# Kernel optimization log

Measured on AMD Instinct MI355X. Metric: run time of the kernel, lower is better.

Reference implementation:

```python
import jax, jax.numpy as jnp
import numpy as np

B, S, D = 1, 2048, 2048
H, G, HD = 32, 8, 64        # n_heads, n_kv_groups, head_dim
GS = H // G                  # group_size
ROPE_BASE = 10000.0


def _rope_tables(seq_len, head_dim):
    inv_freq = 1.0 / (ROPE_BASE ** (jnp.arange(0, head_dim, 2, dtype=jnp.float32) / head_dim))
    angles = jnp.arange(seq_len, dtype=jnp.float32)[:, None] * inv_freq[None, :]  # [S, HD/2]
    angles = jnp.concatenate([angles, angles], axis=-1)                            # [S, HD]
    return jnp.cos(angles), jnp.sin(angles)


def setup_inputs() -> dict:
    key = jax.random.key(0)
    ks = jax.random.split(key, 5)
    x = jax.random.normal(ks[0], (B, S, D), dtype=jnp.float32)
    mask = jnp.triu(jnp.ones((S, S), dtype=bool), k=1)  # True = masked (causal)
    cos_vals, sin_vals = _rope_tables(S, HD)
    scale = 0.02
    Wq = jax.random.normal(ks[1], (H * HD, D), dtype=jnp.float32) * scale
    Wk = jax.random.normal(ks[2], (G * HD, D), dtype=jnp.float32) * scale
    Wv = jax.random.normal(ks[3], (G * HD, D), dtype=jnp.float32) * scale
    Wo = jax.random.normal(ks[4], (D, H * HD), dtype=jnp.float32) * scale
    return {"x": x, "mask": mask, "cos_vals": cos_vals, "sin_vals": sin_vals,
            "Wq": Wq, "Wk": Wk, "Wv": Wv, "Wo": Wo}


def _apply_rope(t, cos, sin):
    # t: [b, heads, S, HD]; cos/sin: [S, HD]
    half = t.shape[-1] // 2
    t1, t2 = t[..., :half], t[..., half:]
    rotated = jnp.concatenate([-t2, t1], axis=-1)
    return t * cos[None, None] + rotated * sin[None, None]


def reference(x, mask, cos_vals, sin_vals, Wq, Wk, Wv, Wo):
    b, s, _ = x.shape
    q = (x @ Wq.T).reshape(b, s, H, HD).transpose(0, 2, 1, 3)   # [b,H,S,HD]
    k = (x @ Wk.T).reshape(b, s, G, HD).transpose(0, 2, 1, 3)   # [b,G,S,HD]
    v = (x @ Wv.T).reshape(b, s, G, HD).transpose(0, 2, 1, 3)   # [b,G,S,HD]
    q = _apply_rope(q, cos_vals, sin_vals)
    k = _apply_rope(k, cos_vals, sin_vals)
    # Group-broadcast instead of repeat_interleave (same math)
    q = q.reshape(b, G, GS, s, HD)
    scores = jnp.einsum('bghqd,bgkd->bghqk', q, k)              # [b,G,GS,S,S]
    scores = jnp.where(mask[None, None, None], -jnp.inf, scores)
    weights = jax.nn.softmax(scores / np.sqrt(HD).astype(np.float32), axis=-1)
    out = jnp.einsum('bghqk,bgkd->bghqd', weights, v)           # [b,G,GS,S,HD]
    out = out.reshape(b, H, s, HD).transpose(0, 2, 1, 3).reshape(b, s, H * HD)
    return out @ Wo.T
```

## Files before the change

### kernel.cpp

```cpp
#include <hip/hip_runtime.h>
#include <cstddef>
#include <cstdint>

#define S 2048
#define Dm 2048
#define NH 32
#define NG 8
#define HD 64

typedef __attribute__((ext_vector_type(8))) short bf16x8;
typedef __attribute__((ext_vector_type(4))) short bf16x4;
typedef __attribute__((ext_vector_type(4))) float f32x4;

__device__ __forceinline__ float fast_exp2(float x) { return __builtin_amdgcn_exp2f(x); }

__device__ __forceinline__ unsigned short f2bf(float f) {
  unsigned int u = __builtin_bit_cast(unsigned int, f);
  u = (u + 0x7fffu + ((u >> 16) & 1u)) >> 16;
  return (unsigned short)u;
}
__device__ __forceinline__ unsigned int pk2bf(float lo, float hi) {
  unsigned int a = __builtin_bit_cast(unsigned int, lo) + 0x8000u;
  unsigned int b = __builtin_bit_cast(unsigned int, hi) + 0x8000u;
  return (a >> 16) | (b & 0xffff0000u);
}
__device__ __forceinline__ void gl_lds16(const unsigned short* g, unsigned short* l) {
  __builtin_amdgcn_global_load_lds(
      (const __attribute__((address_space(1))) unsigned int*)g,
      (__attribute__((address_space(3))) unsigned int*)l, 16, 0, 0);
}

__device__ __forceinline__ void lds_drain_barrier() {
  asm volatile("s_waitcnt lgkmcnt(0)" ::: "memory");
  asm volatile("s_barrier" ::: "memory");
}

#define QSC 0.1803368801111601f

__global__ __launch_bounds__(256) void cvt_all(const float* __restrict__ x,
                                               const float* __restrict__ Wq,
                                               const float* __restrict__ Wk,
                                               const float* __restrict__ Wv,
                                               const float* __restrict__ Wo,
                                               unsigned short* __restrict__ xb,
                                               unsigned short* __restrict__ Wcat,
                                               unsigned short* __restrict__ Wob) {
  int i = blockIdx.x * 256 + threadIdx.x;
  const float4* src;
  ushort4* dst;
  if (i < 1048576)      { src = (const float4*)x  + i;             dst = (ushort4*)xb + i; }
  else if (i < 2097152) { src = (const float4*)Wq + (i - 1048576); dst = (ushort4*)Wcat + (i - 1048576); }
  else if (i < 2359296) { src = (const float4*)Wk + (i - 2097152); dst = (ushort4*)Wcat + 1048576 + (i - 2097152); }
  else if (i < 2621440) { src = (const float4*)Wv + (i - 2359296); dst = (ushort4*)Wcat + 1310720 + (i - 2359296); }
  else                  { src = (const float4*)Wo + (i - 2621440); dst = (ushort4*)Wob + (i - 2621440); }
  float4 v = *src;
  ushort4 o;
  o.x = f2bf(v.x); o.y = f2bf(v.y); o.z = f2bf(v.z); o.w = f2bf(v.w);
  *dst = o;
}

template<int MI, int NJ>
__global__ __launch_bounds__(256) void gemm_bf16(const unsigned short* __restrict__ A,
                                                 const unsigned short* __restrict__ B,
                                                 float* __restrict__ Cf,
                                                 unsigned short* __restrict__ Cb,
                                                 unsigned short* __restrict__ VtOut,
                                                 const float* __restrict__ cosv,
                                                 const float* __restrict__ sinv,
                                                 int M, int N, int K) {
  constexpr int BM = MI * 32, BN = NJ * 32;
  __shared__ __align__(16) unsigned short As[2][BM * 64];
  __shared__ __align__(16) unsigned short Bs[2][BN * 64];
  const int tid = threadIdx.x;
  const int lane = tid & 63, wave = tid >> 6;
  const int row0 = blockIdx.y * BM, col0 = blockIdx.x * BN;
  const int wr = (wave >> 1) * (MI * 16), wc = (wave & 1) * (NJ * 16);
  const int fr = lane & 15, q4 = lane >> 4;

  f32x4 acc[MI][NJ];
#pragma unroll
  for (int i = 0; i < MI; i++)
#pragma unroll
    for (int j = 0; j < NJ; j++) acc[i][j] = (f32x4){0.f, 0.f, 0.f, 0.f};

  const int nk = K >> 6;

  auto stage = [&](int k0, int buf) {
#pragma unroll
    for (int c = 0; c < MI; c++) {
      int p = tid + c * 256;
      int r = p >> 3, sl = ((p & 7) ^ (r & 7)) * 8;
      gl_lds16(&A[(size_t)(row0 + r) * K + k0 + sl], &As[buf][p * 8]);
    }
#pragma unroll
    for (int b = 0; b < NJ; b++) {
      int p = tid + b * 256;
      int r = p >> 3, sl = ((p & 7) ^ (r & 7)) * 8;
      gl_lds16(&B[(size_t)(col0 + r) * K + k0 + sl], &Bs[buf][p * 8]);
    }
  };

  auto compute = [&](const unsigned short* Ab, const unsigned short* Bb) {
#pragma unroll
    for (int kk = 0; kk < 2; kk++) {
      bf16x8 af[MI], bfr[NJ];
#pragma unroll
      for (int i = 0; i < MI; i++) {
        int R = wr + i * 16 + fr;
        af[i] = *(const bf16x8*)&Ab[R * 64 + ((q4 + kk * 4) ^ (R & 7)) * 8];
      }
#pragma unroll
      for (int j = 0; j < NJ; j++) {
        int R = wc + j * 16 + fr;
        bfr[j] = *(const bf16x8*)&Bb[R * 64 + ((q4 + kk * 4) ^ (R & 7)) * 8];
      }
#pragma unroll
      for (int i = 0; i < MI; i++)
#pragma unroll
        for (int j = 0; j < NJ; j++)
          acc[i][j] = __builtin_amdgcn_mfma_f32_16x16x32_bf16(af[i], bfr[j], acc[i][j], 0, 0, 0);
    }
  };

  stage(0, 0);
  stage(64, 1);

  for (int t = 0; t < nk; ++t) {
    if (t + 1 < nk) {
      if constexpr (MI + NJ == 6)      asm volatile("s_waitcnt vmcnt(6)" ::: "memory");
      else if constexpr (MI + NJ == 4) asm volatile("s_waitcnt vmcnt(4)" ::: "memory");
      else                             asm volatile("s_waitcnt vmcnt(8)" ::: "memory");
    } else {
      asm volatile("s_waitcnt vmcnt(0)" ::: "memory");
    }
    asm volatile("s_barrier" ::: "memory");

    compute(As[t & 1], Bs[t & 1]);

    lds_drain_barrier();
    if (t + 2 < nk) stage((t + 2) << 6, t & 1);
  }

  const int cc = lane & 15, cr = (lane >> 4) * 4;

  if (cosv) {
#pragma unroll
    for (int i = 0; i < MI; i++) {
      int grb = row0 + wr + i * 16 + cr;
#pragma unroll
      for (int j = 0; j < 2; j++) {
        int gc = col0 + wc + j * 16 + cc;
        if (gc < 2560) {
          int d = j * 16 + cc;
          float qs = (gc < 2048) ? QSC : 1.0f;
#pragma unroll
          for (int r = 0; r < 4; r++) {
            float c = cosv[(grb + r) * 64 + d];
            float s = sinv[(grb + r) * 64 + d];
            float t1 = acc[i][j][r], t2 = acc[i][j + 2][r];
            acc[i][j][r]     = (t1 * c - t2 * s) * qs;
            acc[i][j + 2][r] = (t2 * c + t1 * s) * qs;
          }
        }
      }
    }
  }

#pragma unroll
  for (int i = 0; i < MI; i++)
#pragma unroll
    for (int j = 0; j < NJ; j++) {
      int gc = col0 + wc + j * 16 + cc;
#pragma unroll
      for (int r = 0; r < 4; r++) {
        int gr = row0 + wr + i * 16 + cr + r;
        if (cosv) {
          if (gc >= 2560) VtOut[(size_t)(gc - 2560) * 2048 + gr] = f2bf(acc[i][j][r]);
          else            Cb[(size_t)gr * N + gc] = f2bf(acc[i][j][r]);
        } else if (Cf)    Cf[(size_t)gr * N + gc] = acc[i][j][r];
        else              Cb[(size_t)gr * N + gc] = f2bf(acc[i][j][r]);
      }
    }
}

__global__ __launch_bounds__(256, 2) void flash_mfma(const unsigned short* __restrict__ QKV,
                                                     const unsigned short* __restrict__ Vt_g,
                                                     unsigned short* __restrict__ Ob) {
  __shared__ __align__(16) unsigned short Ks[2][64 * 64];
  __shared__ __align__(16) unsigned short Vs[2][64 * 64];

  const int tid = threadIdx.x;
  const int lane = tid & 63, wave = tid >> 6;
  const int m15 = lane & 15, q4 = lane >> 4;

  const int L = blockIdx.x;
  const int h = L & 31, g = h >> 2;
  const int u0 = L >> 5, a = u0 >> 3, b = u0 & 7;
  const int u = (a == 0) ? 15 - b : b;
  const int qb = u * 128;
  const int ntiles = 2 * u + 2;

  bf16x8 qf[2][2];
#pragma unroll
  for (int f = 0; f < 2; f++) {
    const size_t qrow = (size_t)(qb + f * 64 + wave * 16 + m15) * 3072 + h * 64;
    qf[f][0] = *(const bf16x8*)&QKV[qrow + q4 * 8];
    qf[f][1] = *(const bf16x8*)&QKV[qrow + 32 + q4 * 8];
  }

  f32x4 accO[2][4];
  float l_lane[2] = {0.f, 0.f};
#pragma unroll
  for (int f = 0; f < 2; f++)
#pragma unroll
    for (int v = 0; v < 4; v++) accO[f][v] = (f32x4){0.f, 0.f, 0.f, 0.f};

  const int p0 = wave * 128 + lane, p1 = p0 + 64;
  const int sr0 = p0 >> 3, so0 = ((p0 & 7) ^ (sr0 & 7)) * 8;
  const int sr1 = p1 >> 3, so1 = ((p1 & 7) ^ (sr1 & 7)) * 8;

#pragma unroll
  for (int t = 0; t < 2; t++) {
    const int k0 = t * 64;
    gl_lds16(&QKV[(size_t)(k0 + sr0) * 3072 + 2048 + g * 64 + so0], &Ks[t][p0 * 8]);
    gl_lds16(&QKV[(size_t)(k0 + sr1) * 3072 + 2048 + g * 64 + so1], &Ks[t][p1 * 8]);
    gl_lds16(&Vt_g[(size_t)(g * 64 + sr0) * 2048 + k0 + so0], &Vs[t][p0 * 8]);
    gl_lds16(&Vt_g[(size_t)(g * 64 + sr1) * 2048 + k0 + so1], &Vs[t][p1 * 8]);
  }

  for (int t = 0; t < ntiles; t++) {
    if (t + 1 < ntiles) asm volatile("s_waitcnt vmcnt(4)" ::: "memory");
    else                asm volatile("s_waitcnt vmcnt(0)" ::: "memory");
    asm volatile("s_barrier" ::: "memory");

    const unsigned short* Kb = Ks[t & 1];
    const unsigned short* Vb = Vs[t & 1];
    const bool act0 = (t < ntiles - 1);

    f32x4 sc[2][4];
#pragma unroll
    for (int kt = 0; kt < 4; kt++) {
      const int krow = kt * 16 + m15;
      bf16x8 kf0 = *(const bf16x8*)&Kb[krow * 64 + (q4 ^ (krow & 7)) * 8];
      bf16x8 kf1 = *(const bf16x8*)&Kb[krow * 64 + ((q4 + 4) ^ (krow & 7)) * 8];
      f32x4 z1 = (f32x4){0.f, 0.f, 0.f, 0.f};
      z1 = __builtin_amdgcn_mfma_f32_16x16x32_bf16(kf0, qf[1][0], z1, 0, 0, 0);
      sc[1][kt] = __builtin_amdgcn_mfma_f32_16x16x32_bf16(kf1, qf[1][1], z1, 0, 0, 0);
      if (act0) {
        f32x4 z0 = (f32x4){0.f, 0.f, 0.f, 0.f};
        z0 = __builtin_amdgcn_mfma_f32_16x16x32_bf16(kf0, qf[0][0], z0, 0, 0, 0);
        sc[0][kt] = __builtin_amdgcn_mfma_f32_16x16x32_bf16(kf1, qf[0][1], z0, 0, 0, 0);
      }
    }

    bf16x8 pA0[2], pA1[2];
#pragma unroll
    for (int f = 0; f < 2; f++) {
      if (f == 0 && !act0) continue;
      if (t == 2 * u + f) {
        const int qo = wave * 16 + m15;
#pragma unroll
        for (int kt = 0; kt < 4; kt++)
#pragma unroll
          for (int r = 0; r < 4; r++)
            if (kt * 16 + q4 * 4 + r > qo) sc[f][kt][r] = -1e30f;
      }
      float rs = 0.f;
#pragma unroll
      for (int kt = 0; kt < 4; kt++)
#pragma unroll
        for (int r = 0; r < 4; r++) {
          float p = fast_exp2(sc[f][kt][r]);
          sc[f][kt][r] = p;
          rs += p;
        }
      l_lane[f] += rs;

      int4 pa0, pa1;
      pa0.x = pk2bf(sc[f][0][0], sc[f][0][1]); pa0.y = pk2bf(sc[f][0][2], sc[f][0][3]);
      pa0.z = pk2bf(sc[f][1][0], sc[f][1][1]); pa0.w = pk2bf(sc[f][1][2], sc[f][1][3]);
      pa1.x = pk2bf(sc[f][2][0], sc[f][2][1]); pa1.y = pk2bf(sc[f][2][2], sc[f][2][3]);
      pa1.z = pk2bf(sc[f][3][0], sc[f][3][1]); pa1.w = pk2bf(sc[f][3][2], sc[f][3][3]);
      pA0[f] = __builtin_bit_cast(bf16x8, pa0);
      pA1[f] = __builtin_bit_cast(bf16x8, pa1);
    }

#pragma unroll
    for (int vt = 0; vt < 4; vt++) {
      const int vrow = vt * 16 + m15;
      const int base = vrow * 64, sw = vrow & 7, half = (q4 & 1) * 4, c1 = q4 >> 1;
      bf16x4 w00 = *(const bf16x4*)&Vb[base + (c1 ^ sw) * 8 + half];
      bf16x4 w01 = *(const bf16x4*)&Vb[base + ((c1 + 2) ^ sw) * 8 + half];
      bf16x4 w10 = *(const bf16x4*)&Vb[base + ((c1 + 4) ^ sw) * 8 + half];
      bf16x4 w11 = *(const bf16x4*)&Vb[base + ((c1 + 6) ^ sw) * 8 + half];
      bf16x8 vB0 = __builtin_shufflevector(w00, w01, 0, 1, 2, 3, 4, 5, 6, 7);
      bf16x8 vB1 = __builtin_shufflevector(w10, w11, 0, 1, 2, 3, 4, 5, 6, 7);
      accO[1][vt] = __builtin_amdgcn_mfma_f32_16x16x32_bf16(pA0[1], vB0, accO[1][vt], 0, 0, 0);
      accO[1][vt] = __builtin_amdgcn_mfma_f32_16x16x32_bf16(pA1[1], vB1, accO[1][vt], 0, 0, 0);
      if (act0) {
        accO[0][vt] = __builtin_amdgcn_mfma_f32_16x16x32_bf16(pA0[0], vB0, accO[0][vt], 0, 0, 0);
        accO[0][vt] = __builtin_amdgcn_mfma_f32_16x16x32_bf16(pA1[0], vB1, accO[0][vt], 0, 0, 0);
      }
    }

    lds_drain_barrier();
    if (t + 2 < ntiles) {
      const int k2 = (t + 2) * 64;
      unsigned short* Kn = (unsigned short*)Ks[t & 1];
      unsigned short* Vn = (unsigned short*)Vs[t & 1];
      gl_lds16(&QKV[(size_t)(k2 + sr0) * 3072 + 2048 + g * 64 + so0], &Kn[p0 * 8]);
      gl_lds16(&QKV[(size_t)(k2 + sr1) * 3072 + 2048 + g * 64 + so1], &Kn[p1 * 8]);
      gl_lds16(&Vt_g[(size_t)(g * 64 + sr0) * 2048 + k2 + so0], &Vn[p0 * 8]);
      gl_lds16(&Vt_g[(size_t)(g * 64 + sr1) * 2048 + k2 + so1], &Vn[p1 * 8]);
    }
  }

#pragma unroll
  for (int f = 0; f < 2; f++) {
    float lsum = l_lane[f];
    lsum += __shfl_xor(lsum, 16);
    lsum += __shfl_xor(lsum, 32);
    float lr[4];
#pragma unroll
    for (int r = 0; r < 4; r++) lr[r] = 1.0f / __shfl(lsum, q4 * 20 + r);
#pragma unroll
    for (int vt = 0; vt < 4; vt++)
#pragma unroll
      for (int r = 0; r < 4; r++) {
        int row = qb + f * 64 + wave * 16 + q4 * 4 + r;
        Ob[(size_t)row * 2048 + h * 64 + vt * 16 + m15] = f2bf(accO[f][vt][r] * lr[r]);
      }
  }
}

extern "C" void kernel_launch(void* const* d_in, const int* in_sizes, int n_in,
                              void* d_out, int out_size, void* d_ws, size_t ws_size,
                              hipStream_t stream) {
  const float* x    = (const float*)d_in[0];
  const float* cosv = (const float*)d_in[2];
  const float* sinv = (const float*)d_in[3];
  const float* Wq   = (const float*)d_in[4];
  const float* Wk   = (const float*)d_in[5];
  const float* Wv   = (const float*)d_in[6];
  const float* Wo   = (const float*)d_in[7];
  float* out = (float*)d_out;

  unsigned short* xb   = (unsigned short*)d_ws;
  unsigned short* Wcat = xb + (size_t)2048 * 2048;
  unsigned short* Wob  = Wcat + (size_t)3072 * 2048;
  unsigned short* QKV  = Wob + (size_t)2048 * 2048;
  unsigned short* Vt_g = QKV + (size_t)3072 * 2048;

  dim3 blk(256);
  cvt_all<<<14336, blk, 0, stream>>>(x, Wq, Wk, Wv, Wo, xb, Wcat, Wob);
  gemm_bf16<2, 4><<<dim3(24, 32), blk, 0, stream>>>(xb, Wcat, nullptr, QKV, Vt_g, cosv, sinv, 2048, 3072, 2048);
  flash_mfma<<<512, blk, 0, stream>>>(QKV, Vt_g, xb);
  gemm_bf16<2, 2><<<dim3(32, 32), blk, 0, stream>>>(xb, Wob, out, nullptr, nullptr, nullptr, nullptr, 2048, 2048, 2048);
}
```

Measured before the change: 216.0 us.

## Split flash attention blocks to one 64-row query tile per block

Each flash-attention block now handles a single 64-row query tile instead of two, so the grid doubles to 1024 blocks. Launch bounds rise to allow 4 blocks per CU, and tiles are ordered heavy-first for causal load balancing. The aim is more parallelism and occupancy with fewer registers per thread. The cost is that each K/V tile loaded into shared memory is now reused by only one query tile instead of two, which doubles K/V global traffic.

```diff
diff --git a/kernel.cpp b/kernel.cpp
--- a/kernel.cpp
+++ b/kernel.cpp
@@ -183,7 +183,7 @@
     }
 }
 
-__global__ __launch_bounds__(256, 2) void flash_mfma(const unsigned short* __restrict__ QKV,
+__global__ __launch_bounds__(256, 4) void flash_mfma(const unsigned short* __restrict__ QKV,
                                                      const unsigned short* __restrict__ Vt_g,
                                                      unsigned short* __restrict__ Ob) {
   __shared__ __align__(16) unsigned short Ks[2][64 * 64];
@@ -195,25 +195,22 @@
 
   const int L = blockIdx.x;
   const int h = L & 31, g = h >> 2;
-  const int u0 = L >> 5, a = u0 >> 3, b = u0 & 7;
-  const int u = (a == 0) ? 15 - b : b;
-  const int qb = u * 128;
-  const int ntiles = 2 * u + 2;
-
-  bf16x8 qf[2][2];
-#pragma unroll
-  for (int f = 0; f < 2; f++) {
-    const size_t qrow = (size_t)(qb + f * 64 + wave * 16 + m15) * 3072 + h * 64;
-    qf[f][0] = *(const bf16x8*)&QKV[qrow + q4 * 8];
-    qf[f][1] = *(const bf16x8*)&QKV[qrow + 32 + q4 * 8];
-  }
-
-  f32x4 accO[2][4];
-  float l_lane[2] = {0.f, 0.f};
-#pragma unroll
-  for (int f = 0; f < 2; f++)
-#pragma unroll
-    for (int v = 0; v < 4; v++) accO[f][v] = (f32x4){0.f, 0.f, 0.f, 0.f};
+  const int u0 = L >> 5, a = u0 >> 4, b = u0 & 15;
+  const int v = (a == 0) ? 31 - b : b;
+  const int qb = v * 64;
+  const int ntiles = v + 1;
+
+  bf16x8 qf0, qf1;
+  {
+    const size_t qrow = (size_t)(qb + wave * 16 + m15) * 3072 + h * 64;
+    qf0 = *(const bf16x8*)&QKV[qrow + q4 * 8];
+    qf1 = *(const bf16x8*)&QKV[qrow + 32 + q4 * 8];
+  }
+
+  f32x4 accO[4];
+  float l_lane = 0.f;
+#pragma unroll
+  for (int vt = 0; vt < 4; vt++) accO[vt] = (f32x4){0.f, 0.f, 0.f, 0.f};
 
   const int p0 = wave * 128 + lane, p1 = p0 + 64;
   const int sr0 = p0 >> 3, so0 = ((p0 & 7) ^ (sr0 & 7)) * 8;
@@ -235,55 +232,45 @@
 
     const unsigned short* Kb = Ks[t & 1];
     const unsigned short* Vb = Vs[t & 1];
-    const bool act0 = (t < ntiles - 1);
-
-    f32x4 sc[2][4];
+
+    f32x4 sc[4];
 #pragma unroll
     for (int kt = 0; kt < 4; kt++) {
       const int krow = kt * 16 + m15;
       bf16x8 kf0 = *(const bf16x8*)&Kb[krow * 64 + (q4 ^ (krow & 7)) * 8];
       bf16x8 kf1 = *(const bf16x8*)&Kb[krow * 64 + ((q4 + 4) ^ (krow & 7)) * 8];
-      f32x4 z1 = (f32x4){0.f, 0.f, 0.f, 0.f};
-      z1 = __builtin_amdgcn_mfma_f32_16x16x32_bf16(kf0, qf[1][0], z1, 0, 0, 0);
-      sc[1][kt] = __builtin_amdgcn_mfma_f32_16x16x32_bf16(kf1, qf[1][1], z1, 0, 0, 0);
-      if (act0) {
-        f32x4 z0 = (f32x4){0.f, 0.f, 0.f, 0.f};
-        z0 = __builtin_amdgcn_mfma_f32_16x16x32_bf16(kf0, qf[0][0], z0, 0, 0, 0);
-        sc[0][kt] = __builtin_amdgcn_mfma_f32_16x16x32_bf16(kf1, qf[0][1], z0, 0, 0, 0);
-      }
-    }
-
-    bf16x8 pA0[2], pA1[2];
-#pragma unroll
-    for (int f = 0; f < 2; f++) {
-      if (f == 0 && !act0) continue;
-      if (t == 2 * u + f) {
-        const int qo = wave * 16 + m15;
-#pragma unroll
-        for (int kt = 0; kt < 4; kt++)
-#pragma unroll
-          for (int r = 0; r < 4; r++)
-            if (kt * 16 + q4 * 4 + r > qo) sc[f][kt][r] = -1e30f;
-      }
-      float rs = 0.f;
+      f32x4 z = (f32x4){0.f, 0.f, 0.f, 0.f};
+      z = __builtin_amdgcn_mfma_f32_16x16x32_bf16(kf0, qf0, z, 0, 0, 0);
+      sc[kt] = __builtin_amdgcn_mfma_f32_16x16x32_bf16(kf1, qf1, z, 0, 0, 0);
+    }
+
+    if (t == v) {
+      const int qo = wave * 16 + m15;
 #pragma unroll
       for (int kt = 0; kt < 4; kt++)
 #pragma unroll
-        for (int r = 0; r < 4; r++) {
-          float p = fast_exp2(sc[f][kt][r]);
-          sc[f][kt][r] = p;
-          rs += p;
-        }
-      l_lane[f] += rs;
-
-      int4 pa0, pa1;
-      pa0.x = pk2bf(sc[f][0][0], sc[f][0][1]); pa0.y = pk2bf(sc[f][0][2], sc[f][0][3]);
-      pa0.z = pk2bf(sc[f][1][0], sc[f][1][1]); pa0.w = pk2bf(sc[f][1][2], sc[f][1][3]);
-      pa1.x = pk2bf(sc[f][2][0], sc[f][2][1]); pa1.y = pk2bf(sc[f][2][2], sc[f][2][3]);
-      pa1.z = pk2bf(sc[f][3][0], sc[f][3][1]); pa1.w = pk2bf(sc[f][3][2], sc[f][3][3]);
-      pA0[f] = __builtin_bit_cast(bf16x8, pa0);
-      pA1[f] = __builtin_bit_cast(bf16x8, pa1);
-    }
+        for (int r = 0; r < 4; r++)
+          if (kt * 16 + q4 * 4 + r > qo) sc[kt][r] = -1e30f;
+    }
+
+    float rs = 0.f;
+#pragma unroll
+    for (int kt = 0; kt < 4; kt++)
+#pragma unroll
+      for (int r = 0; r < 4; r++) {
+        float p = fast_exp2(sc[kt][r]);
+        sc[kt][r] = p;
+        rs += p;
+      }
+    l_lane += rs;
+
+    int4 pa0, pa1;
+    pa0.x = pk2bf(sc[0][0], sc[0][1]); pa0.y = pk2bf(sc[0][2], sc[0][3]);
+    pa0.z = pk2bf(sc[1][0], sc[1][1]); pa0.w = pk2bf(sc[1][2], sc[1][3]);
+    pa1.x = pk2bf(sc[2][0], sc[2][1]); pa1.y = pk2bf(sc[2][2], sc[2][3]);
+    pa1.z = pk2bf(sc[3][0], sc[3][1]); pa1.w = pk2bf(sc[3][2], sc[3][3]);
+    bf16x8 pA0 = __builtin_bit_cast(bf16x8, pa0);
+    bf16x8 pA1 = __builtin_bit_cast(bf16x8, pa1);
 
 #pragma unroll
     for (int vt = 0; vt < 4; vt++) {
@@ -295,12 +282,8 @@
       bf16x4 w11 = *(const bf16x4*)&Vb[base + ((c1 + 6) ^ sw) * 8 + half];
       bf16x8 vB0 = __builtin_shufflevector(w00, w01, 0, 1, 2, 3, 4, 5, 6, 7);
       bf16x8 vB1 = __builtin_shufflevector(w10, w11, 0, 1, 2, 3, 4, 5, 6, 7);
-      accO[1][vt] = __builtin_amdgcn_mfma_f32_16x16x32_bf16(pA0[1], vB0, accO[1][vt], 0, 0, 0);
-      accO[1][vt] = __builtin_amdgcn_mfma_f32_16x16x32_bf16(pA1[1], vB1, accO[1][vt], 0, 0, 0);
-      if (act0) {
-        accO[0][vt] = __builtin_amdgcn_mfma_f32_16x16x32_bf16(pA0[0], vB0, accO[0][vt], 0, 0, 0);
-        accO[0][vt] = __builtin_amdgcn_mfma_f32_16x16x32_bf16(pA1[0], vB1, accO[0][vt], 0, 0, 0);
-      }
+      accO[vt] = __builtin_amdgcn_mfma_f32_16x16x32_bf16(pA0, vB0, accO[vt], 0, 0, 0);
+      accO[vt] = __builtin_amdgcn_mfma_f32_16x16x32_bf16(pA1, vB1, accO[vt], 0, 0, 0);
     }
 
     lds_drain_barrier();
@@ -315,22 +298,19 @@
     }
   }
 
-#pragma unroll
-  for (int f = 0; f < 2; f++) {
-    float lsum = l_lane[f];
-    lsum += __shfl_xor(lsum, 16);
-    lsum += __shfl_xor(lsum, 32);
-    float lr[4];
-#pragma unroll
-    for (int r = 0; r < 4; r++) lr[r] = 1.0f / __shfl(lsum, q4 * 20 + r);
-#pragma unroll
-    for (int vt = 0; vt < 4; vt++)
-#pragma unroll
-      for (int r = 0; r < 4; r++) {
-        int row = qb + f * 64 + wave * 16 + q4 * 4 + r;
-        Ob[(size_t)row * 2048 + h * 64 + vt * 16 + m15] = f2bf(accO[f][vt][r] * lr[r]);
-      }
-  }
+  float lsum = l_lane;
+  lsum += __shfl_xor(lsum, 16);
+  lsum += __shfl_xor(lsum, 32);
+  float lr[4];
+#pragma unroll
+  for (int r = 0; r < 4; r++) lr[r] = 1.0f / __shfl(lsum, q4 * 20 + r);
+#pragma unroll
+  for (int vt = 0; vt < 4; vt++)
+#pragma unroll
+    for (int r = 0; r < 4; r++) {
+      int row = qb + wave * 16 + q4 * 4 + r;
+      Ob[(size_t)row * 2048 + h * 64 + vt * 16 + m15] = f2bf(accO[vt][r] * lr[r]);
+    }
 }
 
 extern "C" void kernel_launch(void* const* d_in, const int* in_sizes, int n_in,
@@ -354,6 +334,6 @@
   dim3 blk(256);
   cvt_all<<<14336, blk, 0, stream>>>(x, Wq, Wk, Wv, Wo, xb, Wcat, Wob);
   gemm_bf16<2, 4><<<dim3(24, 32), blk, 0, stream>>>(xb, Wcat, nullptr, QKV, Vt_g, cosv, sinv, 2048, 3072, 2048);
-  flash_mfma<<<512, blk, 0, stream>>>(QKV, Vt_g, xb);
+  flash_mfma<<<1024, blk, 0, stream>>>(QKV, Vt_g, xb);
   gemm_bf16<2, 2><<<dim3(32, 32), blk, 0, stream>>>(xb, Wob, out, nullptr, nullptr, nullptr, nullptr, 2048, 2048, 2048);
 }
```

Measured after the change: 217.3 us. About the same (+0.6%).
